# Kernel tuning notes

Hardware: AMD Instinct MI355X
Metric: run time of the kernel (lower is better)

## Reference

```python
import jax, jax.numpy as jnp
import numpy as np

B, H, S, D = 2, 8, 4096, 64
TEMPERATURE = 8.0


def setup_inputs() -> dict:
    key = jax.random.key(0)
    kq, kk, kv, km = jax.random.split(key, 4)
    q = jax.random.normal(kq, (B, H, S, D), dtype=jnp.float32)
    k = jax.random.normal(kk, (B, H, S, D), dtype=jnp.float32)
    v = jax.random.normal(kv, (B, H, S, D), dtype=jnp.float32)
    mask = jax.random.randint(km, (1, 1, S, S), 0, 2, dtype=jnp.int32)
    return {"q": q, "k": k, "v": v, "mask": mask}


def reference(q, k, v, mask):
    # scores = q @ k^T / temperature  -> [B,H,S,S]
    scores = jnp.einsum("bhqd,bhkd->bhqk", q, k) / TEMPERATURE
    # masked_fill(mask == 0, -inf)
    scores = jnp.where(mask == 0, -jnp.inf, scores)
    attn = jax.nn.softmax(scores, axis=-1)
    output = jnp.einsum("bhqk,bhkd->bhqd", attn, v)
    return (output, attn)
```

## Files before the change

kernel.cpp:

```cpp
#include <hip/hip_runtime.h>
#include <stdint.h>

typedef __attribute__((ext_vector_type(8))) short short8;
typedef __attribute__((ext_vector_type(4))) float float4v;

#define SEQ 4096
#define HD 64
#define QB 128
#define KT 64
#define HEADS 16
#define NT (SEQ / KT)
#define MWORDS (SEQ / 64)
#define TILE_BYTES 8192
#define QSCALE 0.18033688f

__device__ __forceinline__ ushort f2bf(float f) {
    union { float f; uint32_t u; } x; x.f = f;
    uint32_t u = x.u;
    return (ushort)((u + 0x7FFFu + ((u >> 16) & 1u)) >> 16);
}

__device__ __forceinline__ uint32_t cvt_pk_bf16(float lo, float hi) {
    uint32_t r;
    asm("v_cvt_pk_bf16_f32 %0, %1, %2" : "=v"(r) : "v"(lo), "v"(hi));
    return r;
}

__device__ __forceinline__ float exp2_hw(float x) { return __builtin_amdgcn_exp2f(x); }
__device__ __forceinline__ float log2_hw(float x) { return __builtin_amdgcn_logf(x); }

__device__ __forceinline__ void gload_lds16(const void* g, void* l) {
    __builtin_amdgcn_global_load_lds(
        (const __attribute__((address_space(1))) uint32_t*)g,
        (__attribute__((address_space(3))) uint32_t*)l, 16, 0, 0);
}

__global__ __launch_bounds__(256) void pack_mask_kernel(const int* __restrict__ mask,
                                                        unsigned long long* __restrict__ mb) {
    const int qrow = blockIdx.x;
    const int wave = threadIdx.x >> 6;
    const int lane = threadIdx.x & 63;
    const int* rp = mask + (size_t)qrow * SEQ;
    #pragma unroll
    for (int i = 0; i < 16; ++i) {
        const int widx = wave * 16 + i;
        const int mv = rp[widx * 64 + lane];
        unsigned long long b = __ballot(mv != 0);
        if (lane == 0) mb[(size_t)qrow * MWORDS + widx] = b;
    }
}

__global__ __launch_bounds__(256) void prep_kv_kernel(const float* __restrict__ kg,
                                                      const float* __restrict__ vg,
                                                      char* __restrict__ ktiles,
                                                      char* __restrict__ vtiles) {
    __shared__ __align__(16) float Tl[64][68];
    const int bid = blockIdx.x;
    const int tid = threadIdx.x;
    const float* Kg = kg + (size_t)bid * KT * HD;
    const float* Vg = vg + (size_t)bid * KT * HD;
    char* Kt = ktiles + (size_t)bid * TILE_BYTES;
    char* Vt = vtiles + (size_t)bid * TILE_BYTES;

    {
        const int r = tid >> 2, c0 = (tid & 3) * 16;
        #pragma unroll
        for (int j = 0; j < 4; ++j)
            *(float4v*)&Tl[r][c0 + j * 4] = *(const float4v*)(Kg + r * HD + c0 + j * 4);
    }
    __syncthreads();
    #pragma unroll
    for (int cc = 0; cc < 2; ++cc) {
        const int c = tid + cc * 256;
        const int t = c >> 7, h = (c >> 6) & 1, g = (c >> 4) & 3, li = c & 15;
        const int row = 32 * (t >> 1) + 8 * (li >> 2) + 4 * (t & 1) + (li & 3);
        const float* src = &Tl[row][h * 32 + g * 8];
        short8 w;
        #pragma unroll
        for (int e = 0; e < 8; ++e) w[e] = (short)f2bf(src[e]);
        *(short8*)(Kt + c * 16) = w;
    }
    __syncthreads();
    {
        const int r = tid >> 2, c0 = (tid & 3) * 16;
        #pragma unroll
        for (int j = 0; j < 4; ++j)
            *(float4v*)&Tl[r][c0 + j * 4] = *(const float4v*)(Vg + r * HD + c0 + j * 4);
    }
    __syncthreads();
    #pragma unroll
    for (int cc = 0; cc < 2; ++cc) {
        const int c = tid + cc * 256;
        const int dt = c >> 7, h = (c >> 6) & 1, g = (c >> 4) & 3, li = c & 15;
        short8 w;
        #pragma unroll
        for (int e = 0; e < 8; ++e) w[e] = (short)f2bf(Tl[h * 32 + g * 8 + e][dt * 16 + li]);
        *(short8*)(Vt + c * 16) = w;
    }
}

#define STAGE_K(KTI, DST) do {                                                     \
    const char* _s = Ktile + (size_t)(KTI) * TILE_BYTES + wave * 1024 + lane * 16; \
    gload_lds16(_s, (char*)(DST) + wave * 1024);                                   \
} while (0)

#define STAGE_V(KTI, DST) do {                                                     \
    const char* _s = Vtile + (size_t)(KTI) * TILE_BYTES + wave * 1024 + lane * 16; \
    gload_lds16(_s, (char*)(DST) + wave * 1024);                                   \
} while (0)

__global__ __launch_bounds__(512, 4) void attn_kernel(
    const float* __restrict__ qg, const unsigned long long* __restrict__ mb,
    const char* __restrict__ ktiles, const char* __restrict__ vtiles,
    float* __restrict__ outg, float* __restrict__ attng)
{
    __shared__ __align__(16) char Lds[4][TILE_BYTES];

    const int tid  = threadIdx.x;
    const int wave = tid >> 6;
    const int lane = tid & 63;
    const int g    = lane >> 4;
    const int li   = lane & 15;

    const int bid = blockIdx.x;
    const int blk = (bid & 7) * 64 + (bid >> 3);
    const int bh  = blk >> 5;
    const int qb  = blk & 31;

    const size_t qkvBase = (size_t)bh * SEQ * HD;
    const float* Qg = qg + qkvBase + (size_t)qb * QB * HD;
    const char* Ktile = ktiles + (size_t)bh * NT * TILE_BYTES;
    const char* Vtile = vtiles + (size_t)bh * NT * TILE_BYTES;

    const int wq0 = wave * 16;
    short8 aq[2];
    #pragma unroll
    for (int h = 0; h < 2; ++h) {
        const float* src = Qg + (wq0 + li) * HD + h * 32 + g * 8;
        short8 t;
        #pragma unroll
        for (int e = 0; e < 8; ++e) t[e] = (short)f2bf(src[e] * QSCALE);
        aq[h] = t;
    }

    const int qrow = qb * QB + wq0 + li;
    const unsigned long long* mrow = mb + (size_t)qrow * MWORDS;

    STAGE_K(0, Lds[0]);
    STAGE_K(1, Lds[1]);
    asm volatile("s_waitcnt vmcnt(1)" ::: "memory");
    __builtin_amdgcn_s_barrier();
    asm volatile("" ::: "memory");

    float lsum = 0.f;
    for (int kt = 0; kt < NT; ++kt) {
        if (kt + 2 < NT) STAGE_K(kt + 2, Lds[(kt + 2) % 3]);
        const unsigned long long mw = mrow[kt];
        const uint32_t mlo = (uint32_t)mw >> (g * 8);
        const uint32_t mhi = (uint32_t)(mw >> 32) >> (g * 8);

        const char* Kb = Lds[kt % 3] + lane * 16;
        short8 bk[4][2];
        #pragma unroll
        for (int t = 0; t < 4; ++t)
            #pragma unroll
            for (int h = 0; h < 2; ++h)
                bk[t][h] = *(const short8*)(Kb + (t * 2 + h) * 1024);

        float4v accs[4];
        #pragma unroll
        for (int t = 0; t < 4; ++t) accs[t] = (float4v){0.f, 0.f, 0.f, 0.f};
        __builtin_amdgcn_s_setprio(1);
        #pragma unroll
        for (int t = 0; t < 4; ++t) {
            accs[t] = __builtin_amdgcn_mfma_f32_16x16x32_bf16(bk[t][0], aq[0], accs[t], 0, 0, 0);
            accs[t] = __builtin_amdgcn_mfma_f32_16x16x32_bf16(bk[t][1], aq[1], accs[t], 0, 0, 0);
        }
        __builtin_amdgcn_s_setprio(0);
        const uint32_t nib[4] = { mlo & 0xFu, (mlo >> 4) & 0xFu, mhi & 0xFu, (mhi >> 4) & 0xFu };
        #pragma unroll
        for (int t = 0; t < 4; ++t) {
            #pragma unroll
            for (int r = 0; r < 4; ++r) {
                const float e = exp2_hw(accs[t][r]);
                lsum += ((nib[t] >> r) & 1u) ? e : 0.f;
            }
        }
        if (kt < NT - 2) {
            asm volatile("s_waitcnt vmcnt(2)" ::: "memory");
            __builtin_amdgcn_s_barrier();
            asm volatile("" ::: "memory");
        } else if (kt == NT - 2) {
            asm volatile("s_waitcnt vmcnt(1)" ::: "memory");
            __builtin_amdgcn_s_barrier();
            asm volatile("" ::: "memory");
        }
    }
    lsum += __shfl_xor(lsum, 16);
    lsum += __shfl_xor(lsum, 32);
    const float linv2 = -log2_hw(lsum);

    float* attnT = attng + (size_t)bh * SEQ * SEQ + (size_t)qrow * SEQ + g * 8;
    float4v acco[4];
    #pragma unroll
    for (int dt = 0; dt < 4; ++dt) acco[dt] = (float4v){0.f, 0.f, 0.f, 0.f};

    __syncthreads();
    STAGE_K(0, Lds[0]);
    STAGE_V(0, Lds[2]);
    asm volatile("s_waitcnt vmcnt(0)" ::: "memory");
    __builtin_amdgcn_s_barrier();
    asm volatile("" ::: "memory");

    for (int kt = 0; kt < NT; ++kt) {
        const int b = kt & 1;
        if (kt < NT - 1) { STAGE_K(kt + 1, Lds[b ^ 1]); STAGE_V(kt + 1, Lds[2 + (b ^ 1)]); }
        const unsigned long long mw = mrow[kt];
        __builtin_amdgcn_sched_barrier(0);

        const uint32_t mlo = (uint32_t)mw >> (g * 8);
        const uint32_t mhi = (uint32_t)(mw >> 32) >> (g * 8);

        const char* Kb = Lds[b] + lane * 16;
        const char* Vb = Lds[2 + b] + lane * 16;
        short8 bk[4][2], vb[4][2];
        #pragma unroll
        for (int t = 0; t < 4; ++t)
            #pragma unroll
            for (int h = 0; h < 2; ++h) {
                bk[t][h] = *(const short8*)(Kb + (t * 2 + h) * 1024);
                vb[t][h] = *(const short8*)(Vb + (t * 2 + h) * 1024);
            }

        float4v accs[4];
        #pragma unroll
        for (int t = 0; t < 4; ++t) accs[t] = (float4v){0.f, 0.f, 0.f, 0.f};
        __builtin_amdgcn_s_setprio(1);
        #pragma unroll
        for (int t = 0; t < 4; ++t) {
            accs[t] = __builtin_amdgcn_mfma_f32_16x16x32_bf16(bk[t][0], aq[0], accs[t], 0, 0, 0);
            accs[t] = __builtin_amdgcn_mfma_f32_16x16x32_bf16(bk[t][1], aq[1], accs[t], 0, 0, 0);
        }
        __builtin_amdgcn_s_setprio(0);

        const uint32_t nib[4] = { mlo & 0xFu, (mlo >> 4) & 0xFu, mhi & 0xFu, (mhi >> 4) & 0xFu };
        float4v pv[4];
        #pragma unroll
        for (int t = 0; t < 4; ++t) {
            #pragma unroll
            for (int r = 0; r < 4; ++r) {
                const float e = exp2_hw(accs[t][r] + linv2);
                pv[t][r] = ((nib[t] >> r) & 1u) ? e : 0.f;
            }
        }

        uint32_t pk[4][2];
        #pragma unroll
        for (int t = 0; t < 4; ++t) {
            pk[t][0] = cvt_pk_bf16(pv[t][0], pv[t][1]);
            pk[t][1] = cvt_pk_bf16(pv[t][2], pv[t][3]);
        }
        union { uint32_t u[4]; short8 s; } pa0, pa1;
        pa0.u[0] = pk[0][0]; pa0.u[1] = pk[0][1]; pa0.u[2] = pk[1][0]; pa0.u[3] = pk[1][1];
        pa1.u[0] = pk[2][0]; pa1.u[1] = pk[2][1]; pa1.u[2] = pk[3][0]; pa1.u[3] = pk[3][1];

        __builtin_amdgcn_s_setprio(1);
        #pragma unroll
        for (int dt = 0; dt < 4; ++dt) {
            acco[dt] = __builtin_amdgcn_mfma_f32_16x16x32_bf16(vb[dt][0], pa0.s, acco[dt], 0, 0, 0);
            acco[dt] = __builtin_amdgcn_mfma_f32_16x16x32_bf16(vb[dt][1], pa1.s, acco[dt], 0, 0, 0);
        }
        __builtin_amdgcn_s_setprio(0);

        float* ap = attnT + kt * KT;
        *(float4v*)(ap)      = pv[0];
        *(float4v*)(ap + 4)  = pv[1];
        *(float4v*)(ap + 32) = pv[2];
        *(float4v*)(ap + 36) = pv[3];

        if (kt < NT - 1) {
            asm volatile("s_waitcnt vmcnt(4)" ::: "memory");
            __builtin_amdgcn_s_barrier();
            asm volatile("" ::: "memory");
        }
    }

    float* outW = outg + qkvBase + (size_t)qrow * HD + g * 4;
    #pragma unroll
    for (int dt = 0; dt < 4; ++dt) {
        *(float4v*)(outW + dt * 16) = acco[dt];
    }
}

extern "C" void kernel_launch(void* const* d_in, const int* in_sizes, int n_in,
                              void* d_out, int out_size, void* d_ws, size_t ws_size,
                              hipStream_t stream) {
    (void)in_sizes; (void)n_in; (void)out_size; (void)ws_size;
    const float* q = (const float*)d_in[0];
    const float* k = (const float*)d_in[1];
    const float* v = (const float*)d_in[2];
    const int* mask = (const int*)d_in[3];

    float* outp  = (float*)d_out;
    float* attnp = outp + (size_t)2 * 8 * SEQ * HD;

    char* ws = (char*)d_ws;
    unsigned long long* mb = (unsigned long long*)ws;
    char* ktiles = ws + (size_t)2 * 1024 * 1024;
    char* vtiles = ws + (size_t)10 * 1024 * 1024;

    pack_mask_kernel<<<SEQ, 256, 0, stream>>>(mask, mb);
    prep_kv_kernel<<<HEADS * NT, 256, 0, stream>>>(k, v, ktiles, vtiles);
    attn_kernel<<<HEADS * (SEQ / QB), 512, 0, stream>>>(q, mb, ktiles, vtiles, outp, attnp);
}
```

Baseline: 399.4 us.

## Split softmax row-sum pass into a separate kernel with 32 rows per wave

Moves the first pass, which computes the masked exp-sum normaliser per query row, out of the attention kernel into its own lsum_kernel. That kernel uses 256-thread blocks with two 16-row Q fragments per wave, so each staged K tile feeds twice as many MFMAs. The main kernel then reads the precomputed log-normaliser from a workspace buffer. This adds a kernel launch and a small global round trip, and the main kernel loses the overlap between its two phases in exchange for better K reuse in the sum pass.

Measured after the change: 426.5 us. 1.07x slower.

```diff
diff --git a/kernel.cpp b/kernel.cpp
--- a/kernel.cpp
+++ b/kernel.cpp
@@ -99,22 +99,11 @@
     }
 }
 
-#define STAGE_K(KTI, DST) do {                                                     \
-    const char* _s = Ktile + (size_t)(KTI) * TILE_BYTES + wave * 1024 + lane * 16; \
-    gload_lds16(_s, (char*)(DST) + wave * 1024);                                   \
-} while (0)
-
-#define STAGE_V(KTI, DST) do {                                                     \
-    const char* _s = Vtile + (size_t)(KTI) * TILE_BYTES + wave * 1024 + lane * 16; \
-    gload_lds16(_s, (char*)(DST) + wave * 1024);                                   \
-} while (0)
-
-__global__ __launch_bounds__(512, 4) void attn_kernel(
+__global__ __launch_bounds__(256, 4) void lsum_kernel(
     const float* __restrict__ qg, const unsigned long long* __restrict__ mb,
-    const char* __restrict__ ktiles, const char* __restrict__ vtiles,
-    float* __restrict__ outg, float* __restrict__ attng)
+    const char* __restrict__ ktiles, float* __restrict__ lbuf)
 {
-    __shared__ __align__(16) char Lds[4][TILE_BYTES];
+    __shared__ __align__(16) char Lds3[3][TILE_BYTES];
 
     const int tid  = threadIdx.x;
     const int wave = tid >> 6;
@@ -130,6 +119,126 @@
     const size_t qkvBase = (size_t)bh * SEQ * HD;
     const float* Qg = qg + qkvBase + (size_t)qb * QB * HD;
     const char* Ktile = ktiles + (size_t)bh * NT * TILE_BYTES;
+
+    short8 aq[2][2];
+    #pragma unroll
+    for (int u = 0; u < 2; ++u)
+        #pragma unroll
+        for (int h = 0; h < 2; ++h) {
+            const float* src = Qg + (wave * 32 + u * 16 + li) * HD + h * 32 + g * 8;
+            short8 t;
+            #pragma unroll
+            for (int e = 0; e < 8; ++e) t[e] = (short)f2bf(src[e] * QSCALE);
+            aq[u][h] = t;
+        }
+
+    const int qrow0 = qb * QB + wave * 32 + li;
+    const int qrow1 = qrow0 + 16;
+    const unsigned long long* mrow0 = mb + (size_t)qrow0 * MWORDS;
+    const unsigned long long* mrow1 = mb + (size_t)qrow1 * MWORDS;
+
+#define STAGE_L(KTI, DST) do {                                                      \
+    const char* _s = Ktile + (size_t)(KTI) * TILE_BYTES + wave * 2048 + lane * 16;  \
+    char* _d = (char*)(DST) + wave * 2048;                                          \
+    gload_lds16(_s, _d); gload_lds16(_s + 1024, _d + 1024);                         \
+} while (0)
+
+    STAGE_L(0, Lds3[0]);
+    STAGE_L(1, Lds3[1]);
+    asm volatile("s_waitcnt vmcnt(2)" ::: "memory");
+    __builtin_amdgcn_s_barrier();
+    asm volatile("" ::: "memory");
+
+    float lsum[2] = {0.f, 0.f};
+    for (int kt = 0; kt < NT; ++kt) {
+        if (kt + 2 < NT) STAGE_L(kt + 2, Lds3[(kt + 2) % 3]);
+        const unsigned long long mw0 = mrow0[kt];
+        const unsigned long long mw1 = mrow1[kt];
+
+        const char* Kb = Lds3[kt % 3] + lane * 16;
+        short8 bk[4][2];
+        #pragma unroll
+        for (int t = 0; t < 4; ++t)
+            #pragma unroll
+            for (int h = 0; h < 2; ++h)
+                bk[t][h] = *(const short8*)(Kb + (t * 2 + h) * 1024);
+
+        #pragma unroll
+        for (int u = 0; u < 2; ++u) {
+            const unsigned long long mw = (u == 0) ? mw0 : mw1;
+            float4v accs[4];
+            #pragma unroll
+            for (int t = 0; t < 4; ++t) accs[t] = (float4v){0.f, 0.f, 0.f, 0.f};
+            __builtin_amdgcn_s_setprio(1);
+            #pragma unroll
+            for (int t = 0; t < 4; ++t) {
+                accs[t] = __builtin_amdgcn_mfma_f32_16x16x32_bf16(bk[t][0], aq[u][0], accs[t], 0, 0, 0);
+                accs[t] = __builtin_amdgcn_mfma_f32_16x16x32_bf16(bk[t][1], aq[u][1], accs[t], 0, 0, 0);
+            }
+            __builtin_amdgcn_s_setprio(0);
+            const uint32_t mlo = (uint32_t)mw >> (g * 8);
+            const uint32_t mhi = (uint32_t)(mw >> 32) >> (g * 8);
+            const uint32_t nib[4] = { mlo & 0xFu, (mlo >> 4) & 0xFu, mhi & 0xFu, (mhi >> 4) & 0xFu };
+            float ls = 0.f;
+            #pragma unroll
+            for (int t = 0; t < 4; ++t)
+                #pragma unroll
+                for (int r = 0; r < 4; ++r) {
+                    const float e = exp2_hw(accs[t][r]);
+                    ls += ((nib[t] >> r) & 1u) ? e : 0.f;
+                }
+            lsum[u] += ls;
+        }
+        if (kt < NT - 1) {
+            asm volatile("s_waitcnt vmcnt(2)" ::: "memory");
+            __builtin_amdgcn_s_barrier();
+            asm volatile("" ::: "memory");
+        }
+    }
+
+    float* lb = lbuf + ((size_t)bh << 12);
+    #pragma unroll
+    for (int u = 0; u < 2; ++u) {
+        float s = lsum[u];
+        s += __shfl_xor(s, 16);
+        s += __shfl_xor(s, 32);
+        if (g == 0) lb[(u == 0) ? qrow0 : qrow1] = -log2_hw(s);
+    }
+#undef STAGE_L
+}
+
+#define STAGE_K(KTI, DST) do {                                                     \
+    const char* _s = Ktile + (size_t)(KTI) * TILE_BYTES + wave * 1024 + lane * 16; \
+    gload_lds16(_s, (char*)(DST) + wave * 1024);                                   \
+} while (0)
+
+#define STAGE_V(KTI, DST) do {                                                     \
+    const char* _s = Vtile + (size_t)(KTI) * TILE_BYTES + wave * 1024 + lane * 16; \
+    gload_lds16(_s, (char*)(DST) + wave * 1024);                                   \
+} while (0)
+
+__global__ __launch_bounds__(512, 4) void attn_kernel(
+    const float* __restrict__ qg, const unsigned long long* __restrict__ mb,
+    const char* __restrict__ ktiles, const char* __restrict__ vtiles,
+    const float* __restrict__ lbuf,
+    float* __restrict__ outg, float* __restrict__ attng)
+{
+    __shared__ __align__(16) char Lds[4][TILE_BYTES];
+
+    const int tid  = threadIdx.x;
+    const int wave = tid >> 6;
+    const int lane = tid & 63;
+    const int g    = lane >> 4;
+    const int li   = lane & 15;
+
+    const int bid = blockIdx.x;
+    const int blk = (bid & 7) * 64 + (bid >> 3);
+    const int bh  = blk >> 5;
+    const int qb  = blk & 31;
+
+    const size_t qkvBase = (size_t)bh * SEQ * HD;
+    const float* Qg = qg + qkvBase + (size_t)qb * QB * HD;
+    const char* Ktile = ktiles + (size_t)bh * NT * TILE_BYTES;
     const char* Vtile = vtiles + (size_t)bh * NT * TILE_BYTES;
 
     const int wq0 = wave * 16;
@@ -145,67 +254,13 @@
 
     const int qrow = qb * QB + wq0 + li;
     const unsigned long long* mrow = mb + (size_t)qrow * MWORDS;
-
-    STAGE_K(0, Lds[0]);
-    STAGE_K(1, Lds[1]);
-    asm volatile("s_waitcnt vmcnt(1)" ::: "memory");
-    __builtin_amdgcn_s_barrier();
-    asm volatile("" ::: "memory");
-
-    float lsum = 0.f;
-    for (int kt = 0; kt < NT; ++kt) {
-        if (kt + 2 < NT) STAGE_K(kt + 2, Lds[(kt + 2) % 3]);
-        const unsigned long long mw = mrow[kt];
-        const uint32_t mlo = (uint32_t)mw >> (g * 8);
-        const uint32_t mhi = (uint32_t)(mw >> 32) >> (g * 8);
-
-        const char* Kb = Lds[kt % 3] + lane * 16;
-        short8 bk[4][2];
-        #pragma unroll
-        for (int t = 0; t < 4; ++t)
-            #pragma unroll
-            for (int h = 0; h < 2; ++h)
-                bk[t][h] = *(const short8*)(Kb + (t * 2 + h) * 1024);
-
-        float4v accs[4];
-        #pragma unroll
-        for (int t = 0; t < 4; ++t) accs[t] = (float4v){0.f, 0.f, 0.f, 0.f};
-        __builtin_amdgcn_s_setprio(1);
-        #pragma unroll
-        for (int t = 0; t < 4; ++t) {
-            accs[t] = __builtin_amdgcn_mfma_f32_16x16x32_bf16(bk[t][0], aq[0], accs[t], 0, 0, 0);
-            accs[t] = __builtin_amdgcn_mfma_f32_16x16x32_bf16(bk[t][1], aq[1], accs[t], 0, 0, 0);
-        }
-        __builtin_amdgcn_s_setprio(0);
-        const uint32_t nib[4] = { mlo & 0xFu, (mlo >> 4) & 0xFu, mhi & 0xFu, (mhi >> 4) & 0xFu };
-        #pragma unroll
-        for (int t = 0; t < 4; ++t) {
-            #pragma unroll
-            for (int r = 0; r < 4; ++r) {
-                const float e = exp2_hw(accs[t][r]);
-                lsum += ((nib[t] >> r) & 1u) ? e : 0.f;
-            }
-        }
-        if (kt < NT - 2) {
-            asm volatile("s_waitcnt vmcnt(2)" ::: "memory");
-            __builtin_amdgcn_s_barrier();
-            asm volatile("" ::: "memory");
-        } else if (kt == NT - 2) {
-            asm volatile("s_waitcnt vmcnt(1)" ::: "memory");
-            __builtin_amdgcn_s_barrier();
-            asm volatile("" ::: "memory");
-        }
-    }
-    lsum += __shfl_xor(lsum, 16);
-    lsum += __shfl_xor(lsum, 32);
-    const float linv2 = -log2_hw(lsum);
+    const float linv2 = lbuf[((size_t)bh << 12) + qrow];
 
     float* attnT = attng + (size_t)bh * SEQ * SEQ + (size_t)qrow * SEQ + g * 8;
     float4v acco[4];
     #pragma unroll
     for (int dt = 0; dt < 4; ++dt) acco[dt] = (float4v){0.f, 0.f, 0.f, 0.f};
 
-    __syncthreads();
     STAGE_K(0, Lds[0]);
     STAGE_V(0, Lds[2]);
     asm volatile("s_waitcnt vmcnt(0)" ::: "memory");
@@ -308,8 +363,10 @@
     unsigned long long* mb = (unsigned long long*)ws;
     char* ktiles = ws + (size_t)2 * 1024 * 1024;
     char* vtiles = ws + (size_t)10 * 1024 * 1024;
+    float* lbuf  = (float*)(ws + (size_t)18 * 1024 * 1024);
 
     pack_mask_kernel<<<SEQ, 256, 0, stream>>>(mask, mb);
     prep_kv_kernel<<<HEADS * NT, 256, 0, stream>>>(k, v, ktiles, vtiles);
-    attn_kernel<<<HEADS * (SEQ / QB), 512, 0, stream>>>(q, mb, ktiles, vtiles, outp, attnp);
-}
+    lsum_kernel<<<HEADS * (SEQ / QB), 256, 0, stream>>>(q, mb, ktiles, lbuf);
+    attn_kernel<<<HEADS * (SEQ / QB), 512, 0, stream>>>(q, mb, ktiles, vtiles, lbuf, outp, attnp);
+}
```

## Ping-pong even/odd waves between QK and softmax/PV phases in second pass

Applied to the files above, without the earlier changes.

Restructures the second attention pass into a slot schedule in which even and odd waves alternate: one group runs the QK^T MFMAs while the other does the exp, mask, attn store and PV MFMAs, so matrix and vector work from different waves can overlap. K/V staging moves into separate 4-deep LDS rings loaded only by even waves, two tiles ahead, and the mask word is prefetched one tile early. This doubles LDS usage (64KB per block), which may limit occupancy under launch_bounds(512,4), and adds a barrier per half-slot.

Measured after the change: 383.3 us (median of 2 runs). 1.04x faster.

```diff
diff --git a/kernel.cpp b/kernel.cpp
--- a/kernel.cpp
+++ b/kernel.cpp
@@ -99,14 +99,21 @@
     }
 }
 
-#define STAGE_K(KTI, DST) do {                                                     \
+#define STAGE_K8(KTI, DST) do {                                                    \
     const char* _s = Ktile + (size_t)(KTI) * TILE_BYTES + wave * 1024 + lane * 16; \
     gload_lds16(_s, (char*)(DST) + wave * 1024);                                   \
 } while (0)
 
-#define STAGE_V(KTI, DST) do {                                                     \
-    const char* _s = Vtile + (size_t)(KTI) * TILE_BYTES + wave * 1024 + lane * 16; \
-    gload_lds16(_s, (char*)(DST) + wave * 1024);                                   \
+#define STAGE2_K(KTI) do {                                                              \
+    const char* _s = Ktile + (size_t)(KTI) * TILE_BYTES + ew * 2048 + lane * 16;        \
+    char* _d = (char*)LdsK[(KTI) & 3] + ew * 2048;                                      \
+    gload_lds16(_s, _d); gload_lds16(_s + 1024, _d + 1024);                             \
+} while (0)
+
+#define STAGE2_V(KTI) do {                                                              \
+    const char* _s = Vtile + (size_t)(KTI) * TILE_BYTES + ew * 2048 + lane * 16;        \
+    char* _d = (char*)LdsV[(KTI) & 3] + ew * 2048;                                      \
+    gload_lds16(_s, _d); gload_lds16(_s + 1024, _d + 1024);                             \
 } while (0)
 
 __global__ __launch_bounds__(512, 4) void attn_kernel(
@@ -114,7 +121,8 @@
     const char* __restrict__ ktiles, const char* __restrict__ vtiles,
     float* __restrict__ outg, float* __restrict__ attng)
 {
-    __shared__ __align__(16) char Lds[4][TILE_BYTES];
+    __shared__ __align__(16) char LdsK[4][TILE_BYTES];
+    __shared__ __align__(16) char LdsV[4][TILE_BYTES];
 
     const int tid  = threadIdx.x;
     const int wave = tid >> 6;
@@ -146,20 +154,20 @@
     const int qrow = qb * QB + wq0 + li;
     const unsigned long long* mrow = mb + (size_t)qrow * MWORDS;
 
-    STAGE_K(0, Lds[0]);
-    STAGE_K(1, Lds[1]);
+    STAGE_K8(0, LdsK[0]);
+    STAGE_K8(1, LdsK[1]);
     asm volatile("s_waitcnt vmcnt(1)" ::: "memory");
     __builtin_amdgcn_s_barrier();
     asm volatile("" ::: "memory");
 
     float lsum = 0.f;
     for (int kt = 0; kt < NT; ++kt) {
-        if (kt + 2 < NT) STAGE_K(kt + 2, Lds[(kt + 2) % 3]);
+        if (kt + 2 < NT) STAGE_K8(kt + 2, LdsK[(kt + 2) % 3]);
         const unsigned long long mw = mrow[kt];
         const uint32_t mlo = (uint32_t)mw >> (g * 8);
         const uint32_t mhi = (uint32_t)(mw >> 32) >> (g * 8);
 
-        const char* Kb = Lds[kt % 3] + lane * 16;
+        const char* Kb = LdsK[kt % 3] + lane * 16;
         short8 bk[4][2];
         #pragma unroll
         for (int t = 0; t < 4; ++t)
@@ -205,81 +213,102 @@
     #pragma unroll
     for (int dt = 0; dt < 4; ++dt) acco[dt] = (float4v){0.f, 0.f, 0.f, 0.f};
 
+    const int odd = wave & 1;
+    const int ew  = wave >> 1;
+
     __syncthreads();
-    STAGE_K(0, Lds[0]);
-    STAGE_V(0, Lds[2]);
-    asm volatile("s_waitcnt vmcnt(0)" ::: "memory");
+    unsigned long long mwreg = mrow[0];
+    if (!odd) {
+        STAGE2_K(0); STAGE2_V(0);
+        STAGE2_K(1); STAGE2_V(1);
+        asm volatile("s_waitcnt vmcnt(0)" ::: "memory");
+    }
     __builtin_amdgcn_s_barrier();
     asm volatile("" ::: "memory");
 
-    for (int kt = 0; kt < NT; ++kt) {
-        const int b = kt & 1;
-        if (kt < NT - 1) { STAGE_K(kt + 1, Lds[b ^ 1]); STAGE_V(kt + 1, Lds[2 + (b ^ 1)]); }
-        const unsigned long long mw = mrow[kt];
-        __builtin_amdgcn_sched_barrier(0);
-
-        const uint32_t mlo = (uint32_t)mw >> (g * 8);
-        const uint32_t mhi = (uint32_t)(mw >> 32) >> (g * 8);
-
-        const char* Kb = Lds[b] + lane * 16;
-        const char* Vb = Lds[2 + b] + lane * 16;
-        short8 bk[4][2], vb[4][2];
-        #pragma unroll
-        for (int t = 0; t < 4; ++t)
-            #pragma unroll
-            for (int h = 0; h < 2; ++h) {
-                bk[t][h] = *(const short8*)(Kb + (t * 2 + h) * 1024);
-                vb[t][h] = *(const short8*)(Vb + (t * 2 + h) * 1024);
+    float4v accs[4];
+    for (int slot = 0; slot < 2 * NT + 1; ++slot) {
+        const int half = slot & 1;
+        int t_qk = -1, t_fin = -1;
+        if (!odd) {
+            if (!half) { const int t = slot >> 1; if (t < NT) t_qk = t; }
+            else       t_fin = slot >> 1;
+        } else {
+            if (half)  t_qk = slot >> 1;
+            else if (slot > 0) t_fin = (slot >> 1) - 1;
+        }
+
+        if (t_qk >= 0) {
+            if (!odd && t_qk + 2 < NT) { STAGE2_K(t_qk + 2); STAGE2_V(t_qk + 2); }
+            const char* Kb = LdsK[t_qk & 3] + lane * 16;
+            short8 bk[4][2];
+            #pragma unroll
+            for (int t = 0; t < 4; ++t)
+                #pragma unroll
+                for (int h = 0; h < 2; ++h)
+                    bk[t][h] = *(const short8*)(Kb + (t * 2 + h) * 1024);
+            #pragma unroll
+            for (int t = 0; t < 4; ++t) accs[t] = (float4v){0.f, 0.f, 0.f, 0.f};
+            __builtin_amdgcn_s_setprio(1);
+            #pragma unroll
+            for (int t = 0; t < 4; ++t) {
+                accs[t] = __builtin_amdgcn_mfma_f32_16x16x32_bf16(bk[t][0], aq[0], accs[t], 0, 0, 0);
+                accs[t] = __builtin_amdgcn_mfma_f32_16x16x32_bf16(bk[t][1], aq[1], accs[t], 0, 0, 0);
             }
-
-        float4v accs[4];
-        #pragma unroll
-        for (int t = 0; t < 4; ++t) accs[t] = (float4v){0.f, 0.f, 0.f, 0.f};
-        __builtin_amdgcn_s_setprio(1);
-        #pragma unroll
-        for (int t = 0; t < 4; ++t) {
-            accs[t] = __builtin_amdgcn_mfma_f32_16x16x32_bf16(bk[t][0], aq[0], accs[t], 0, 0, 0);
-            accs[t] = __builtin_amdgcn_mfma_f32_16x16x32_bf16(bk[t][1], aq[1], accs[t], 0, 0, 0);
-        }
-        __builtin_amdgcn_s_setprio(0);
-
-        const uint32_t nib[4] = { mlo & 0xFu, (mlo >> 4) & 0xFu, mhi & 0xFu, (mhi >> 4) & 0xFu };
-        float4v pv[4];
-        #pragma unroll
-        for (int t = 0; t < 4; ++t) {
-            #pragma unroll
-            for (int r = 0; r < 4; ++r) {
-                const float e = exp2_hw(accs[t][r] + linv2);
-                pv[t][r] = ((nib[t] >> r) & 1u) ? e : 0.f;
+            __builtin_amdgcn_s_setprio(0);
+        }
+
+        if (t_fin >= 0) {
+            const char* Vb = LdsV[t_fin & 3] + lane * 16;
+            short8 vb[4][2];
+            #pragma unroll
+            for (int t = 0; t < 4; ++t)
+                #pragma unroll
+                for (int h = 0; h < 2; ++h)
+                    vb[t][h] = *(const short8*)(Vb + (t * 2 + h) * 1024);
+
+            const uint32_t mlo = (uint32_t)mwreg >> (g * 8);
+            const uint32_t mhi = (uint32_t)(mwreg >> 32) >> (g * 8);
+            const uint32_t nib[4] = { mlo & 0xFu, (mlo >> 4) & 0xFu, mhi & 0xFu, (mhi >> 4) & 0xFu };
+            float4v pv[4];
+            #pragma unroll
+            for (int t = 0; t < 4; ++t)
+                #pragma unroll
+                for (int r = 0; r < 4; ++r) {
+                    const float e = exp2_hw(accs[t][r] + linv2);
+                    pv[t][r] = ((nib[t] >> r) & 1u) ? e : 0.f;
+                }
+
+            float* ap = attnT + t_fin * KT;
+            *(float4v*)(ap)      = pv[0];
+            *(float4v*)(ap + 4)  = pv[1];
+            *(float4v*)(ap + 32) = pv[2];
+            *(float4v*)(ap + 36) = pv[3];
+
+            if (t_fin + 1 < NT) mwreg = mrow[t_fin + 1];
+
+            uint32_t pk[4][2];
+            #pragma unroll
+            for (int t = 0; t < 4; ++t) {
+                pk[t][0] = cvt_pk_bf16(pv[t][0], pv[t][1]);
+                pk[t][1] = cvt_pk_bf16(pv[t][2], pv[t][3]);
             }
-        }
-
-        uint32_t pk[4][2];
-        #pragma unroll
-        for (int t = 0; t < 4; ++t) {
-            pk[t][0] = cvt_pk_bf16(pv[t][0], pv[t][1]);
-            pk[t][1] = cvt_pk_bf16(pv[t][2], pv[t][3]);
-        }
-        union { uint32_t u[4]; short8 s; } pa0, pa1;
-        pa0.u[0] = pk[0][0]; pa0.u[1] = pk[0][1]; pa0.u[2] = pk[1][0]; pa0.u[3] = pk[1][1];
-        pa1.u[0] = pk[2][0]; pa1.u[1] = pk[2][1]; pa1.u[2] = pk[3][0]; pa1.u[3] = pk[3][1];
-
-        __builtin_amdgcn_s_setprio(1);
-        #pragma unroll
-        for (int dt = 0; dt < 4; ++dt) {
-            acco[dt] = __builtin_amdgcn_mfma_f32_16x16x32_bf16(vb[dt][0], pa0.s, acco[dt], 0, 0, 0);
-            acco[dt] = __builtin_amdgcn_mfma_f32_16x16x32_bf16(vb[dt][1], pa1.s, acco[dt], 0, 0, 0);
-        }
-        __builtin_amdgcn_s_setprio(0);
-
-        float* ap = attnT + kt * KT;
-        *(float4v*)(ap)      = pv[0];
-        *(float4v*)(ap + 4)  = pv[1];
-        *(float4v*)(ap + 32) = pv[2];
-        *(float4v*)(ap + 36) = pv[3];
-
-        if (kt < NT - 1) {
-            asm volatile("s_waitcnt vmcnt(4)" ::: "memory");
+            union { uint32_t u[4]; short8 s; } pa0, pa1;
+            pa0.u[0] = pk[0][0]; pa0.u[1] = pk[0][1]; pa0.u[2] = pk[1][0]; pa0.u[3] = pk[1][1];
+            pa1.u[0] = pk[2][0]; pa1.u[1] = pk[2][1]; pa1.u[2] = pk[3][0]; pa1.u[3] = pk[3][1];
+
+            __builtin_amdgcn_s_setprio(1);
+            #pragma unroll
+            for (int dt = 0; dt < 4; ++dt) {
+                acco[dt] = __builtin_amdgcn_mfma_f32_16x16x32_bf16(vb[dt][0], pa0.s, acco[dt], 0, 0, 0);
+                acco[dt] = __builtin_amdgcn_mfma_f32_16x16x32_bf16(vb[dt][1], pa1.s, acco[dt], 0, 0, 0);
+            }
+            __builtin_amdgcn_s_setprio(0);
+        }
+
+        if (slot < 2 * NT) {
+            if (t_qk >= 0 || t_fin >= 0)
+                asm volatile("s_waitcnt vmcnt(5)" ::: "memory");
             __builtin_amdgcn_s_barrier();
             asm volatile("" ::: "memory");
         }
```
